# Kernel tuning notes

Measured on AMD Instinct MI355X. Metric: run time of the kernel, lower is better.

The kernel has to match this reference:

```python
import jax, jax.numpy as jnp
import numpy as np

B, T, C, HS = 4, 2048, 1024, 64

def setup_inputs() -> dict:
    key = jax.random.key(0)
    k1, k2, k3, k4 = jax.random.split(key, 4)
    # weights stored as [n_embd, head_size] so projection is x @ W
    scale = C ** -0.5
    return {
        "x": jax.random.normal(k1, (B, T, C), dtype=jnp.float32),
        "Wq": jax.random.normal(k2, (C, HS), dtype=jnp.float32) * scale,
        "Wk": jax.random.normal(k3, (C, HS), dtype=jnp.float32) * scale,
        "Wv": jax.random.normal(k4, (C, HS), dtype=jnp.float32) * scale,
    }

def reference(x, Wq, Wk, Wv):
    # single-head causal attention: softmax(QK^T / sqrt(hs)) V, dropout p=0 (eval)
    q = x @ Wq  # [B,T,hs]
    k = x @ Wk
    v = x @ Wv
    hs = k.shape[-1]
    wei = jnp.einsum('bqh,bkh->bqk', q, k) * (hs ** -0.5)  # [B,T,T]
    causal = jnp.tril(jnp.ones((q.shape[1], q.shape[1]), dtype=bool))
    wei = jnp.where(causal[None, :, :], wei, -jnp.inf)
    wei = jax.nn.softmax(wei, axis=-1)
    out = jnp.einsum('bqk,bkh->bqh', wei, v)  # [B,T,hs]
    return out
```

## Files before the change

### kernel.cpp

```cpp
#include <hip/hip_runtime.h>
#include <stdint.h>

#define NB 4
#define NT 2048
#define NC 1024
#define NH 64
#define NM (NB*NT)

typedef unsigned short u16;
typedef unsigned int u32;
typedef __bf16 bf16_t;
typedef float f32x4 __attribute__((ext_vector_type(4)));
typedef bf16_t bf16x8 __attribute__((ext_vector_type(8)));
typedef u16 u16x8 __attribute__((ext_vector_type(8)));
typedef u16 u16x4 __attribute__((ext_vector_type(4)));

__device__ __forceinline__ u16 f2b(float f) {
  return __builtin_bit_cast(u16, (bf16_t)f);
}

__device__ __forceinline__ void gl16(const void* g, void* l) {
  __builtin_amdgcn_global_load_lds(
      (const __attribute__((address_space(1))) u32*)g,
      (__attribute__((address_space(3))) u32*)l, 16, 0, 0);
}

__global__ __launch_bounds__(256) void wt_kernel(const float* __restrict__ Wq,
                                                 const float* __restrict__ Wk,
                                                 const float* __restrict__ Wv,
                                                 u16* __restrict__ wt) {
  __shared__ float t[64][65];
  const int m = blockIdx.x >> 4;
  const int kt = blockIdx.x & 15;
  const int k0 = kt * 64;
  const float* W = (m == 0) ? Wq : (m == 1) ? Wk : Wv;
  {
    const int r = threadIdx.x >> 2, c4 = threadIdx.x & 3;
    #pragma unroll
    for (int j = 0; j < 4; ++j) {
      const float4 f = *(const float4*)(W + (size_t)(k0 + r) * NH + c4 * 16 + j * 4);
      t[r][c4 * 16 + j * 4 + 0] = f.x;
      t[r][c4 * 16 + j * 4 + 1] = f.y;
      t[r][c4 * 16 + j * 4 + 2] = f.z;
      t[r][c4 * 16 + j * 4 + 3] = f.w;
    }
  }
  __syncthreads();
  const int n = threadIdx.x >> 2, kc = threadIdx.x & 3;
  u16x8 a, b;
  #pragma unroll
  for (int j = 0; j < 8; ++j) a[j] = f2b(t[kc * 16 + j][n]);
  #pragma unroll
  for (int j = 0; j < 8; ++j) b[j] = f2b(t[kc * 16 + 8 + j][n]);
  u16* dst = wt + ((size_t)(m * 64 + n)) * NC + k0 + kc * 16;
  *(u16x8*)dst = a;
  *(u16x8*)(dst + 8) = b;
}

__global__ __launch_bounds__(256) void proj_kernel(const float* __restrict__ x,
                                                   const u16* __restrict__ wt,
                                                   u16* __restrict__ qo,
                                                   u16* __restrict__ ko,
                                                   u16* __restrict__ vto) {
  __shared__ float fA[2][16 * 64];
  __shared__ u16 sB[2][64 * 64];
  const int tid = threadIdx.x;
  const int lane = tid & 63;
  const int w = tid >> 6;
  const int g = lane >> 4;
  const int li = lane & 15;
  const int row0 = blockIdx.x * 16;
  const int m = blockIdx.y;
  const int wbase = tid & 0xC0;
  const u16* wslice = wt + (size_t)m * 64 * NC;

  const f32x4 zero = {0.f, 0.f, 0.f, 0.f};
  f32x4 acc = zero;

  const int ar = tid >> 4;
  const int ac = tid & 15;
  const float* asrc0 = x + (size_t)(row0 + ar) * NC + ((ac ^ (ar & 7)) * 4);

  auto stage = [&](int kt, int nxt) {
    const int k0 = kt * 64;
    gl16(asrc0 + k0, (char*)fA[nxt] + wbase * 16);
    #pragma unroll
    for (int j = 0; j < 2; ++j) {
      const int cid = j * 256 + tid;
      const int n = cid >> 3, c = cid & 7;
      gl16(wslice + (size_t)n * NC + k0 + ((c ^ (n & 7)) * 8),
           (char*)sB[nxt] + (j * 4096 + wbase * 16));
    }
  };

  stage(0, 0);
  __syncthreads();

  for (int kt = 0; kt < 16; ++kt) {
    const int cur = kt & 1;
    if (kt < 15) stage(kt + 1, cur ^ 1);
    #pragma unroll
    for (int ks = 0; ks < 2; ++ks) {
      const int c0 = ks * 8 + g * 2;
      const f32x4 a0 = *(const f32x4*)&fA[cur][li * 64 + ((c0 ^ (li & 7)) * 4)];
      const f32x4 a1 = *(const f32x4*)&fA[cur][li * 64 + (((c0 + 1) ^ (li & 7)) * 4)];
      bf16x8 a;
      a[0]=(bf16_t)a0.x; a[1]=(bf16_t)a0.y; a[2]=(bf16_t)a0.z; a[3]=(bf16_t)a0.w;
      a[4]=(bf16_t)a1.x; a[5]=(bf16_t)a1.y; a[6]=(bf16_t)a1.z; a[7]=(bf16_t)a1.w;
      const int n = w * 16 + li;
      const bf16x8 b = *(const bf16x8*)&sB[cur][n * 64 + (((ks * 4 + g) ^ (n & 7)) * 8)];
      acc = __builtin_amdgcn_mfma_f32_16x16x32_bf16(a, b, acc, 0, 0, 0);
    }
    __syncthreads();
  }

  const int rr0 = row0 + g * 4;
  if (m == 0) {
    #pragma unroll
    for (int i = 0; i < 4; ++i)
      qo[(size_t)(rr0 + i) * NH + w * 16 + li] = f2b(acc[i]);
  } else if (m == 1) {
    #pragma unroll
    for (int i = 0; i < 4; ++i)
      ko[(size_t)(rr0 + i) * NH + w * 16 + li] = f2b(acc[i]);
  } else {
    u16x4 pv;
    #pragma unroll
    for (int i = 0; i < 4; ++i) pv[i] = f2b(acc[i]);
    const int hs = w * 16 + li;
    const int bidx = rr0 >> 11;
    const int tt = rr0 & 2047;
    const int tile = tt >> 6, off = tt & 63;
    *(u16x4*)&vto[(((size_t)(bidx * 32 + tile) * 64) + hs) * 64 + off] = pv;
  }
}

struct AttnGrp {
  union {
    struct { u16 K[2][32 * 64]; u16 V[2][64 * 32]; } st;
    struct { float mo[2][16][64]; float ml[2][16]; } mg;
  } u;
};

__global__ __launch_bounds__(512) void attn_kernel(const u16* __restrict__ qg,
                                                   const u16* __restrict__ kg,
                                                   const u16* __restrict__ vtg,
                                                   float* __restrict__ out) {
  __shared__ AttnGrp grp[8];
  __shared__ u16 sP[8][16 * 32];
  const int tid = threadIdx.x;
  const int lane = tid & 63;
  const int s = tid >> 3 >> 3;
  const int g = lane >> 4;
  const int li = lane & 15;
  const int jA = blockIdx.x & 63;
  const int bb = blockIdx.x >> 6;
  const int jB = 127 - jA;
  const size_t bt0 = (size_t)bb * NT;
  const int q0A = jA * 16, q0B = jB * 16;
  const int n1 = (jA >> 1) + 1;

  bf16x8 aqA[2], aqB[2];
  #pragma unroll
  for (int ks = 0; ks < 2; ++ks) {
    aqA[ks] = *(const bf16x8*)(qg + (bt0 + q0A + li) * NH + ks * 32 + g * 8);
    aqB[ks] = *(const bf16x8*)(qg + (bt0 + q0B + li) * NH + ks * 32 + g * 8);
  }

  const f32x4 zero = {0.f, 0.f, 0.f, 0.f};
  f32x4 oA[4], oB[4];
  float lA[4], lB[4];
  #pragma unroll
  for (int i = 0; i < 4; ++i) { oA[i] = zero; oB[i] = zero; lA[i] = 0.f; lB[i] = 0.f; }

  auto stage = [&](int v, int b) {
    const int kvt = (v < n1) ? v : v - n1;
    const size_t kbase = bt0 + (size_t)kvt * 32;
    #pragma unroll
    for (int jj = 0; jj < 4; ++jj) {
      const int idx = jj * 64 + lane;
      const int n = idx >> 3, c = idx & 7;
      gl16(kg + (kbase + n) * NH + ((c ^ (n & 7)) * 8),
           (char*)grp[s].u.st.K[b] + jj * 1024);
    }
    const size_t vbase = ((size_t)(bb * 32 + (kvt >> 1))) * 64;
    const int hoff = (kvt & 1) * 32;
    #pragma unroll
    for (int jj = 0; jj < 4; ++jj) {
      const int idx = jj * 64 + lane;
      const int n = idx >> 2, c = idx & 3;
      gl16(vtg + (vbase + n) * 64 + hoff + ((c ^ (n & 3) ^ ((n >> 2) & 3)) * 8),
           (char*)grp[s].u.st.V[b] + jj * 1024);
    }
  };

  auto computeT = [&](const bf16x8 (&aq)[2], f32x4 (&o)[4], float (&ls)[4],
                      int q0, int kv0, int b) {
    f32x4 sc2[2] = {zero, zero};
    #pragma unroll
    for (int ks = 0; ks < 2; ++ks) {
      #pragma unroll
      for (int fn = 0; fn < 2; ++fn) {
        const int n = fn * 16 + li;
        const bf16x8 bk = *(const bf16x8*)&grp[s].u.st.K[b][n * 64 + (((ks * 4 + g) ^ (n & 7)) * 8)];
        sc2[fn] = __builtin_amdgcn_mfma_f32_16x16x32_bf16(aq[ks], bk, sc2[fn], 0, 0, 0);
      }
    }
    const bool needmask = (kv0 + 31 > q0);
    #pragma unroll
    for (int fn = 0; fn < 2; ++fn) {
      #pragma unroll
      for (int i = 0; i < 4; ++i) {
        const int q = g * 4 + i;
        float v = sc2[fn][i] * 0.125f;
        if (needmask && (kv0 + fn * 16 + li > q0 + q)) v = -1e30f;
        const float e = __expf(v);
        ls[i] += e;
        const int kc = fn * 2 + (li >> 3);
        sP[s][q * 32 + ((kc ^ (q & 3) ^ ((q >> 2) & 3)) * 8) + (li & 7)] = f2b(e);
      }
    }
    const bf16x8 pa = *(const bf16x8*)&sP[s][li * 32 + ((g ^ (li & 3) ^ ((li >> 2) & 3)) * 8)];
    #pragma unroll
    for (int fn = 0; fn < 4; ++fn) {
      const int n = fn * 16 + li;
      const bf16x8 bv = *(const bf16x8*)&grp[s].u.st.V[b][n * 32 + ((g ^ (n & 3) ^ ((n >> 2) & 3)) * 8)];
      o[fn] = __builtin_amdgcn_mfma_f32_16x16x32_bf16(pa, bv, o[fn], 0, 0, 0);
    }
  };

  const int nt = (64 - s) / 8 + 1;
  int v = s;
  stage(v, 0);
  for (int k = 0; k < nt; ++k) {
    if (k + 1 < nt) {
      stage(v + 8, (k + 1) & 1);
      asm volatile("s_waitcnt vmcnt(8)" ::: "memory");
    } else {
      asm volatile("s_waitcnt vmcnt(0)" ::: "memory");
    }
    const int b = k & 1;
    if (v < n1) computeT(aqA, oA, lA, q0A, v * 32, b);
    else        computeT(aqB, oB, lB, q0B, (v - n1) * 32, b);
    v += 8;
  }

  #pragma unroll
  for (int i = 0; i < 4; ++i) {
    float a = lA[i], c = lB[i];
    a += __shfl_xor(a, 1); c += __shfl_xor(c, 1);
    a += __shfl_xor(a, 2); c += __shfl_xor(c, 2);
    a += __shfl_xor(a, 4); c += __shfl_xor(c, 4);
    a += __shfl_xor(a, 8); c += __shfl_xor(c, 8);
    lA[i] = a; lB[i] = c;
  }

  #pragma unroll
  for (int fn = 0; fn < 4; ++fn) {
    #pragma unroll
    for (int i = 0; i < 4; ++i) {
      grp[s].u.mg.mo[0][g * 4 + i][fn * 16 + li] = oA[fn][i];
      grp[s].u.mg.mo[1][g * 4 + i][fn * 16 + li] = oB[fn][i];
    }
  }
  if (li == 0) {
    #pragma unroll
    for (int i = 0; i < 4; ++i) {
      grp[s].u.mg.ml[0][g * 4 + i] = lA[i];
      grp[s].u.mg.ml[1][g * 4 + i] = lB[i];
    }
  }
  __syncthreads();

  {
    const int base = tid * 4;
    const int tile = base >> 10;
    const int r = (base >> 6) & 15;
    const int c0 = base & 63;
    float L = 0.f;
    f32x4 acc = zero;
    #pragma unroll
    for (int s8 = 0; s8 < 8; ++s8) {
      L += grp[s8].u.mg.ml[tile][r];
      acc += *(const f32x4*)&grp[s8].u.mg.mo[tile][r][c0];
    }
    const int row = (tile ? q0B : q0A) + r;
    const float inv = 1.f / L;
    acc *= inv;
    *(f32x4*)&out[(bt0 + row) * NH + c0] = acc;
  }
}

extern "C" void kernel_launch(void* const* d_in, const int* in_sizes, int n_in,
                              void* d_out, int out_size, void* d_ws, size_t ws_size,
                              hipStream_t stream) {
  (void)in_sizes; (void)n_in; (void)out_size; (void)ws_size;
  const float* x  = (const float*)d_in[0];
  const float* Wq = (const float*)d_in[1];
  const float* Wk = (const float*)d_in[2];
  const float* Wv = (const float*)d_in[3];
  float* out = (float*)d_out;
  char* ws = (char*)d_ws;
  u16* qb  = (u16*)(ws);
  u16* kb  = (u16*)(ws + (1u << 20));
  u16* vtb = (u16*)(ws + (2u << 20));
  u16* wtb = (u16*)(ws + (3u << 20));
  hipLaunchKernelGGL(wt_kernel,   dim3(48),      dim3(256), 0, stream, Wq, Wk, Wv, wtb);
  hipLaunchKernelGGL(proj_kernel, dim3(512, 3),  dim3(256), 0, stream, x, wtb, qb, kb, vtb);
  hipLaunchKernelGGL(attn_kernel, dim3(256),     dim3(512), 0, stream, qb, kb, vtb, out);
}
```

Before: 37.59 us.

## Retile QKV projection to 32-row blocks with 32-wide K steps

Result: slower. 40.63 us (+8.1%).

```diff
diff --git a/kernel.cpp b/kernel.cpp
--- a/kernel.cpp
+++ b/kernel.cpp
@@ -57,81 +57,83 @@
   *(u16x8*)(dst + 8) = b;
 }
 
-__global__ __launch_bounds__(256) void proj_kernel(const float* __restrict__ x,
-                                                   const u16* __restrict__ wt,
-                                                   u16* __restrict__ qo,
-                                                   u16* __restrict__ ko,
-                                                   u16* __restrict__ vto) {
-  __shared__ float fA[2][16 * 64];
-  __shared__ u16 sB[2][64 * 64];
+__global__ __launch_bounds__(256, 4) void proj_kernel(const float* __restrict__ x,
+                                                      const u16* __restrict__ wt,
+                                                      u16* __restrict__ qo,
+                                                      u16* __restrict__ ko,
+                                                      u16* __restrict__ vto) {
+  __shared__ float fA[2][32 * 32];
+  __shared__ u16 sB2[2][64 * 32];
   const int tid = threadIdx.x;
   const int lane = tid & 63;
   const int w = tid >> 6;
   const int g = lane >> 4;
   const int li = lane & 15;
-  const int row0 = blockIdx.x * 16;
+  const int row0 = blockIdx.x * 32;
   const int m = blockIdx.y;
   const int wbase = tid & 0xC0;
   const u16* wslice = wt + (size_t)m * 64 * NC;
 
   const f32x4 zero = {0.f, 0.f, 0.f, 0.f};
-  f32x4 acc = zero;
-
-  const int ar = tid >> 4;
-  const int ac = tid & 15;
-  const float* asrc0 = x + (size_t)(row0 + ar) * NC + ((ac ^ (ar & 7)) * 4);
-
-  auto stage = [&](int kt, int nxt) {
-    const int k0 = kt * 64;
-    gl16(asrc0 + k0, (char*)fA[nxt] + wbase * 16);
-    #pragma unroll
-    for (int j = 0; j < 2; ++j) {
-      const int cid = j * 256 + tid;
-      const int n = cid >> 3, c = cid & 7;
-      gl16(wslice + (size_t)n * NC + k0 + ((c ^ (n & 7)) * 8),
-           (char*)sB[nxt] + (j * 4096 + wbase * 16));
-    }
+  f32x4 acc[2];
+  acc[0] = zero; acc[1] = zero;
+
+  const int arow = tid >> 3, ach = tid & 7;
+  const int brow = tid >> 2, bch = tid & 3;
+  const float* asrc = x + (size_t)(row0 + arow) * NC + ((ach ^ (arow & 7)) * 4);
+  const u16* bsrc = wslice + (size_t)brow * NC + ((bch ^ (brow & 3)) * 8);
+
+  auto stage = [&](int kt, int buf) {
+    const int k0 = kt * 32;
+    gl16(asrc + k0, (char*)fA[buf] + wbase * 16);
+    gl16(bsrc + k0, (char*)sB2[buf] + wbase * 16);
   };
 
   stage(0, 0);
   __syncthreads();
 
-  for (int kt = 0; kt < 16; ++kt) {
+  for (int kt = 0; kt < 32; ++kt) {
     const int cur = kt & 1;
-    if (kt < 15) stage(kt + 1, cur ^ 1);
-    #pragma unroll
-    for (int ks = 0; ks < 2; ++ks) {
-      const int c0 = ks * 8 + g * 2;
-      const f32x4 a0 = *(const f32x4*)&fA[cur][li * 64 + ((c0 ^ (li & 7)) * 4)];
-      const f32x4 a1 = *(const f32x4*)&fA[cur][li * 64 + (((c0 + 1) ^ (li & 7)) * 4)];
-      bf16x8 a;
-      a[0]=(bf16_t)a0.x; a[1]=(bf16_t)a0.y; a[2]=(bf16_t)a0.z; a[3]=(bf16_t)a0.w;
-      a[4]=(bf16_t)a1.x; a[5]=(bf16_t)a1.y; a[6]=(bf16_t)a1.z; a[7]=(bf16_t)a1.w;
-      const int n = w * 16 + li;
-      const bf16x8 b = *(const bf16x8*)&sB[cur][n * 64 + (((ks * 4 + g) ^ (n & 7)) * 8)];
-      acc = __builtin_amdgcn_mfma_f32_16x16x32_bf16(a, b, acc, 0, 0, 0);
-    }
+    if (kt < 31) stage(kt + 1, cur ^ 1);
+    bf16x8 aF[2];
+    #pragma unroll
+    for (int rt = 0; rt < 2; ++rt) {
+      const int r = rt * 16 + li;
+      const f32x4 a0 = *(const f32x4*)&fA[cur][r * 32 + (((2 * g) ^ (r & 7)) * 4)];
+      const f32x4 a1 = *(const f32x4*)&fA[cur][r * 32 + (((2 * g + 1) ^ (r & 7)) * 4)];
+      bf16x8 v;
+      v[0]=(bf16_t)a0.x; v[1]=(bf16_t)a0.y; v[2]=(bf16_t)a0.z; v[3]=(bf16_t)a0.w;
+      v[4]=(bf16_t)a1.x; v[5]=(bf16_t)a1.y; v[6]=(bf16_t)a1.z; v[7]=(bf16_t)a1.w;
+      aF[rt] = v;
+    }
+    const int n = w * 16 + li;
+    const bf16x8 bF = *(const bf16x8*)&sB2[cur][n * 32 + ((g ^ (n & 3)) * 8)];
+    acc[0] = __builtin_amdgcn_mfma_f32_16x16x32_bf16(aF[0], bF, acc[0], 0, 0, 0);
+    acc[1] = __builtin_amdgcn_mfma_f32_16x16x32_bf16(aF[1], bF, acc[1], 0, 0, 0);
     __syncthreads();
   }
 
-  const int rr0 = row0 + g * 4;
-  if (m == 0) {
-    #pragma unroll
-    for (int i = 0; i < 4; ++i)
-      qo[(size_t)(rr0 + i) * NH + w * 16 + li] = f2b(acc[i]);
-  } else if (m == 1) {
-    #pragma unroll
-    for (int i = 0; i < 4; ++i)
-      ko[(size_t)(rr0 + i) * NH + w * 16 + li] = f2b(acc[i]);
-  } else {
-    u16x4 pv;
-    #pragma unroll
-    for (int i = 0; i < 4; ++i) pv[i] = f2b(acc[i]);
-    const int hs = w * 16 + li;
-    const int bidx = rr0 >> 11;
-    const int tt = rr0 & 2047;
-    const int tile = tt >> 6, off = tt & 63;
-    *(u16x4*)&vto[(((size_t)(bidx * 32 + tile) * 64) + hs) * 64 + off] = pv;
+  #pragma unroll
+  for (int rt = 0; rt < 2; ++rt) {
+    const int rr0 = row0 + rt * 16 + g * 4;
+    if (m == 0) {
+      #pragma unroll
+      for (int i = 0; i < 4; ++i)
+        qo[(size_t)(rr0 + i) * NH + w * 16 + li] = f2b(acc[rt][i]);
+    } else if (m == 1) {
+      #pragma unroll
+      for (int i = 0; i < 4; ++i)
+        ko[(size_t)(rr0 + i) * NH + w * 16 + li] = f2b(acc[rt][i]);
+    } else {
+      u16x4 pv;
+      #pragma unroll
+      for (int i = 0; i < 4; ++i) pv[i] = f2b(acc[rt][i]);
+      const int hs = w * 16 + li;
+      const int bidx = rr0 >> 11;
+      const int tt = rr0 & 2047;
+      const int tile = tt >> 6, off = tt & 63;
+      *(u16x4*)&vto[(((size_t)(bidx * 32 + tile) * 64) + hs) * 64 + off] = pv;
+    }
   }
 }
 
@@ -150,7 +152,7 @@
   __shared__ u16 sP[8][16 * 32];
   const int tid = threadIdx.x;
   const int lane = tid & 63;
-  const int s = tid >> 3 >> 3;
+  const int s = tid >> 6;
   const int g = lane >> 4;
   const int li = lane & 15;
   const int jA = blockIdx.x & 63;
@@ -159,6 +161,7 @@
   const size_t bt0 = (size_t)bb * NT;
   const int q0A = jA * 16, q0B = jB * 16;
   const int n1 = (jA >> 1) + 1;
+  const int nB = 64 - (jA >> 1);
 
   bf16x8 aqA[2], aqB[2];
   #pragma unroll
@@ -173,7 +176,7 @@
   #pragma unroll
   for (int i = 0; i < 4; ++i) { oA[i] = zero; oB[i] = zero; lA[i] = 0.f; lB[i] = 0.f; }
 
-  auto stage = [&](int v, int b) {
+  auto stageKV = [&](int v, int b) {
     const int kvt = (v < n1) ? v : v - n1;
     const size_t kbase = bt0 + (size_t)kvt * 32;
     #pragma unroll
@@ -231,10 +234,10 @@
 
   const int nt = (64 - s) / 8 + 1;
   int v = s;
-  stage(v, 0);
+  stageKV(v, 0);
   for (int k = 0; k < nt; ++k) {
     if (k + 1 < nt) {
-      stage(v + 8, (k + 1) & 1);
+      stageKV(v + 8, (k + 1) & 1);
       asm volatile("s_waitcnt vmcnt(8)" ::: "memory");
     } else {
       asm volatile("s_waitcnt vmcnt(0)" ::: "memory");
@@ -305,7 +308,7 @@
   u16* kb  = (u16*)(ws + (1u << 20));
   u16* vtb = (u16*)(ws + (2u << 20));
   u16* wtb = (u16*)(ws + (3u << 20));
-  hipLaunchKernelGGL(wt_kernel,   dim3(48),      dim3(256), 0, stream, Wq, Wk, Wv, wtb);
-  hipLaunchKernelGGL(proj_kernel, dim3(512, 3),  dim3(256), 0, stream, x, wtb, qb, kb, vtb);
-  hipLaunchKernelGGL(attn_kernel, dim3(256),     dim3(512), 0, stream, qb, kb, vtb, out);
-}
+  hipLaunchKernelGGL(wt_kernel,   dim3(48),     dim3(256), 0, stream, Wq, Wk, Wv, wtb);
+  hipLaunchKernelGGL(proj_kernel, dim3(256, 3), dim3(256), 0, stream, x, wtb, qb, kb, vtb);
+  hipLaunchKernelGGL(attn_kernel, dim3(256),    dim3(512), 0, stream, qb, kb, vtb, out);
+}
```
